# Performance work log

Measured on AMD Instinct MI355X. Metric: run time of the kernel, lower is better.

Reference implementation:

```python
import jax, jax.numpy as jnp
import numpy as np

D_MODEL = 256
N_HEADS = 8
N_LEVELS = 4
N_POINTS = 4
D_FFN = 1024
HW = 128
LQ = HW * HW
LIN = N_LEVELS * LQ
BATCH = 2
HEAD_DIM = D_MODEL // N_HEADS
SPATIAL = [(HW, HW)] * N_LEVELS  # static (H, W) per level
EPS = 1e-5


def _layer_norm(x, g, b):
    m = jnp.mean(x, axis=-1, keepdims=True)
    v = jnp.mean(jnp.square(x - m), axis=-1, keepdims=True)
    return (x - m) * jax.lax.rsqrt(v + EPS) * g + b


def _gather(v, idx):
    # v: (N, heads, HW, hd); idx: (N, heads, Lq, P) -> (N, heads, Lq, P, hd)
    N, Hh, Lq, P = idx.shape
    out = jnp.take_along_axis(v, idx.reshape(N, Hh, Lq * P)[..., None], axis=2)
    return out.reshape(N, Hh, Lq, P, -1)


def _ms_deform_attn_core(value, loc, attn):
    # value: (N, Lin, heads, hd); loc: (N, Lq, heads, L, P, 2) in [0,1]; attn: (N, Lq, heads, L, P)
    N, _, Hh, hd = value.shape
    Lq = loc.shape[1]
    out = jnp.zeros((N, Hh, Lq, hd), value.dtype)
    start = 0
    for l, (H, W) in enumerate(SPATIAL):
        v = value[:, start:start + H * W].transpose(0, 2, 1, 3)  # (N, heads, H*W, hd)
        start += H * W
        ll = loc[:, :, :, l].transpose(0, 2, 1, 3, 4)  # (N, heads, Lq, P, 2)
        # F.grid_sample(align_corners=False, padding_mode='zeros') on grid 2*loc-1:
        # pixel coord = loc * size - 0.5
        x = ll[..., 0] * W - 0.5
        y = ll[..., 1] * H - 0.5
        x0 = jnp.floor(x)
        y0 = jnp.floor(y)
        wx = x - x0
        wy = y - y0
        x0i = x0.astype(jnp.int32)
        y0i = y0.astype(jnp.int32)
        acc = jnp.zeros((N, Hh, Lq, N_POINTS, hd), value.dtype)
        for dy, wyc in ((0, 1.0 - wy), (1, wy)):
            for dx, wxc in ((0, 1.0 - wx), (1, wx)):
                xi = x0i + dx
                yi = y0i + dy
                valid = (xi >= 0) & (xi < W) & (yi >= 0) & (yi < H)
                idx = jnp.clip(yi, 0, H - 1) * W + jnp.clip(xi, 0, W - 1)
                g = _gather(v, idx)
                w = (wxc * wyc * valid).astype(value.dtype)
                acc = acc + g * w[..., None]
        aw = attn[:, :, :, l].transpose(0, 2, 1, 3)  # (N, heads, Lq, P)
        out = out + jnp.sum(acc * aw[..., None], axis=3)
    return out.transpose(0, 2, 1, 3).reshape(N, Lq, Hh * hd)


def _forward(cur_src, src_all, pos, reference_points, spatial_shape,
             W_off, b_off, W_attn, b_attn, W_val, b_val, W_out, b_out,
             gamma1, beta1, W1, b1, W2, b2, gamma2, beta2):
    N, Lq, d = cur_src.shape
    q = cur_src + pos[:, -1]                      # with_pos_embed(cur_src, pos[-1])
    inp = src_all + pos.reshape(N, -1, d)         # with_pos_embed(src_all, cat(pos, 1))
    value = (inp @ W_val + b_val).reshape(N, -1, N_HEADS, HEAD_DIM)
    off = (q @ W_off + b_off).reshape(N, Lq, N_HEADS, N_LEVELS, N_POINTS, 2)
    attn = (q @ W_attn + b_attn).reshape(N, Lq, N_HEADS, N_LEVELS * N_POINTS)
    attn = jax.nn.softmax(attn, axis=-1).reshape(N, Lq, N_HEADS, N_LEVELS, N_POINTS)
    # offset_normalizer = stack([W, H], -1)
    normalizer = jnp.stack([spatial_shape[..., 1], spatial_shape[..., 0]], -1).astype(cur_src.dtype)
    loc = reference_points[:, :, None, :, None, :] + off / normalizer[None, None, None, :, None, :]
    src2 = _ms_deform_attn_core(value, loc, attn) @ W_out + b_out
    src = _layer_norm(cur_src + src2, gamma1, beta1)   # dropout is identity in eval
    ffn = jax.nn.relu(src @ W1 + b1) @ W2 + b2
    return _layer_norm(src + ffn, gamma2, beta2)


def setup_inputs():
    key = jax.random.key(0)
    ks = jax.random.split(key, 16)
    s = 0.02
    f32 = jnp.float32
    return {
        "cur_src": jax.random.normal(ks[0], (BATCH, LQ, D_MODEL), f32),
        "src_all": jax.random.normal(ks[1], (BATCH, LIN, D_MODEL), f32),
        "pos": jax.random.normal(ks[2], (BATCH, N_LEVELS, LQ, D_MODEL), f32),
        "reference_points": jax.random.uniform(ks[3], (BATCH, LQ, N_LEVELS, 2), f32),
        "spatial_shape": jnp.array(SPATIAL, dtype=jnp.int32),
        "level_start_index": (jnp.arange(N_LEVELS) * LQ).astype(jnp.int32),
        "W_off": jax.random.normal(ks[4], (D_MODEL, N_HEADS * N_LEVELS * N_POINTS * 2), f32) * s,
        "b_off": jax.random.normal(ks[5], (N_HEADS * N_LEVELS * N_POINTS * 2,), f32) * 0.5,
        "W_attn": jax.random.normal(ks[6], (D_MODEL, N_HEADS * N_LEVELS * N_POINTS), f32) * s,
        "b_attn": jnp.zeros((N_HEADS * N_LEVELS * N_POINTS,), f32),
        "W_val": jax.random.normal(ks[7], (D_MODEL, D_MODEL), f32) * s,
        "b_val": jnp.zeros((D_MODEL,), f32),
        "W_out": jax.random.normal(ks[8], (D_MODEL, D_MODEL), f32) * s,
        "b_out": jnp.zeros((D_MODEL,), f32),
        "gamma1": jnp.ones((D_MODEL,), f32),
        "beta1": jnp.zeros((D_MODEL,), f32),
        "W1": jax.random.normal(ks[9], (D_MODEL, D_FFN), f32) * s,
        "b1": jnp.zeros((D_FFN,), f32),
        "W2": jax.random.normal(ks[10], (D_FFN, D_MODEL), f32) * s,
        "b2": jnp.zeros((D_MODEL,), f32),
        "gamma2": jnp.ones((D_MODEL,), f32),
        "beta2": jnp.zeros((D_MODEL,), f32),
    }


def reference(cur_src, src_all, pos, reference_points, spatial_shape, level_start_index,
              W_off, b_off, W_attn, b_attn, W_val, b_val, W_out, b_out,
              gamma1, beta1, W1, b1, W2, b2, gamma2, beta2):
    return _forward(cur_src, src_all, pos, reference_points, spatial_shape,
                    W_off, b_off, W_attn, b_attn, W_val, b_val, W_out, b_out,
                    gamma1, beta1, W1, b1, W2, b2, gamma2, beta2)
```

## Files before the change

kernel.cpp:

```cpp
#include <hip/hip_runtime.h>

#define LQN   16384
#define LINN  65536

typedef __attribute__((ext_vector_type(8))) short bf16x8;
typedef __attribute__((ext_vector_type(4))) float f32x4;
typedef __attribute__((ext_vector_type(4))) unsigned short bf16x4;

__device__ __forceinline__ unsigned short f2bf(float f) {
  unsigned u = __float_as_uint(f);
  u += 0x7FFFu + ((u >> 16) & 1u);
  return (unsigned short)(u >> 16);
}

__global__ __launch_bounds__(256) void wtrans_kernel(const float* __restrict__ W,
                                                     unsigned short* __restrict__ Wt,
                                                     int K, int N) {
  int idx = blockIdx.x * 256 + threadIdx.x;
  int n = idx / K, k = idx - n * K;
  Wt[idx] = f2bf(W[(size_t)k * N + n]);
}

__global__ __launch_bounds__(256) void q_kernel(const float* __restrict__ cur,
                                                const float* __restrict__ pos,
                                                unsigned short* __restrict__ q) {
  size_t i = (size_t)blockIdx.x * 256 + threadIdx.x;
  size_t row = i >> 6;
  int n = (int)(row >> 14), lq = (int)(row & 16383);
  float4 a = ((const float4*)cur)[i];
  float4 b = ((const float4*)pos)[(((size_t)n * 4 + 3) * LQN + lq) * 64 + (i & 63)];
  bf16x4 o;
  o.x = f2bf(a.x + b.x); o.y = f2bf(a.y + b.y);
  o.z = f2bf(a.z + b.z); o.w = f2bf(a.w + b.w);
  ((bf16x4*)q)[i] = o;
}

template <int A_BF16, int HAS_A2, int DO_RELU, int OUT_BF16>
__global__ __launch_bounds__(256) void gemm_kernel(
    const void* __restrict__ Ap, const float* __restrict__ A2,
    const unsigned short* __restrict__ Bt, const float* __restrict__ bias,
    void* __restrict__ Cp, int M, int N, int K) {
  __shared__ unsigned short As[128][72];
  __shared__ unsigned short Bs[128][72];
  const int tid = threadIdx.x;
  const int m0 = blockIdx.x * 128, n0 = blockIdx.y * 128;
  const int wave = tid >> 6, lane = tid & 63;
  const int wm = (wave >> 1) * 64, wn = (wave & 1) * 64;
  const int l15 = lane & 15, quad = lane >> 4;

  f32x4 acc[4][4];
#pragma unroll
  for (int i = 0; i < 4; i++)
#pragma unroll
    for (int j = 0; j < 4; j++)
#pragma unroll
      for (int r = 0; r < 4; r++) acc[i][j][r] = 0.f;

  for (int k0 = 0; k0 < K; k0 += 64) {
    if (A_BF16) {
      const unsigned short* A = (const unsigned short*)Ap;
#pragma unroll
      for (int j = 0; j < 4; j++) {
        int c = tid + j * 256;
        int row = c >> 3, ks = (c & 7) * 8;
        bf16x8 v = *(const bf16x8*)(A + (size_t)(m0 + row) * K + k0 + ks);
        *(bf16x8*)&As[row][ks] = v;
      }
    } else {
      const float* A = (const float*)Ap;
#pragma unroll
      for (int j = 0; j < 8; j++) {
        int c = tid + j * 256;
        int row = c >> 4, ks = (c & 15) * 4;
        float4 v = *(const float4*)(A + (size_t)(m0 + row) * K + k0 + ks);
        if (HAS_A2) {
          float4 w = *(const float4*)(A2 + (size_t)(m0 + row) * K + k0 + ks);
          v.x += w.x; v.y += w.y; v.z += w.z; v.w += w.w;
        }
        bf16x4 b;
        b.x = f2bf(v.x); b.y = f2bf(v.y); b.z = f2bf(v.z); b.w = f2bf(v.w);
        *(bf16x4*)&As[row][ks] = b;
      }
    }
#pragma unroll
    for (int j = 0; j < 4; j++) {
      int c = tid + j * 256;
      int row = c >> 3, ks = (c & 7) * 8;
      bf16x8 v = *(const bf16x8*)(Bt + (size_t)(n0 + row) * K + k0 + ks);
      *(bf16x8*)&Bs[row][ks] = v;
    }
    __syncthreads();
#pragma unroll
    for (int kk = 0; kk < 64; kk += 32) {
      bf16x8 af[4], bfr[4];
#pragma unroll
      for (int i = 0; i < 4; i++) af[i] = *(const bf16x8*)&As[wm + i * 16 + l15][kk + quad * 8];
#pragma unroll
      for (int j = 0; j < 4; j++) bfr[j] = *(const bf16x8*)&Bs[wn + j * 16 + l15][kk + quad * 8];
#pragma unroll
      for (int i = 0; i < 4; i++)
#pragma unroll
        for (int j = 0; j < 4; j++)
          acc[i][j] = __builtin_amdgcn_mfma_f32_16x16x32_bf16(af[i], bfr[j], acc[i][j], 0, 0, 0);
    }
    __syncthreads();
  }
#pragma unroll
  for (int i = 0; i < 4; i++) {
#pragma unroll
    for (int j = 0; j < 4; j++) {
      const int col = n0 + wn + j * 16 + l15;
      const float bv = bias[col];
#pragma unroll
      for (int r = 0; r < 4; r++) {
        const int row = m0 + wm + i * 16 + quad * 4 + r;
        float v = acc[i][j][r] + bv;
        if (DO_RELU) v = fmaxf(v, 0.f);
        if (OUT_BF16)
          ((unsigned short*)Cp)[(size_t)row * N + col] = f2bf(v);
        else
          ((float*)Cp)[(size_t)row * N + col] = v;
      }
    }
  }
}

__global__ __launch_bounds__(256) void sample_kernel(
    const unsigned short* __restrict__ value, const float* __restrict__ offs,
    const float* __restrict__ attnl, const float* __restrict__ refp,
    unsigned int* __restrict__ attn_out) {
  const int tid = threadIdx.x;
  const int sub = tid >> 4;
  const int c = tid & 15;
  const int g = blockIdx.x * 16 + sub;
  const int n = g >> 17;
  const int nl = g >> 3;
  const int h = g & 7;

  const float* lg = attnl + (size_t)nl * 128 + h * 16;
  float e[16];
  float mx = -1e30f;
#pragma unroll
  for (int i = 0; i < 16; i++) { e[i] = lg[i]; mx = fmaxf(mx, e[i]); }
  float s = 0.f;
#pragma unroll
  for (int i = 0; i < 16; i++) { e[i] = __expf(e[i] - mx); s += e[i]; }
  const float inv = 1.f / s;

  const int pt = c;
  const int pl = pt >> 2;
  const float ox = offs[((size_t)g * 16 + pt) * 2 + 0];
  const float oy = offs[((size_t)g * 16 + pt) * 2 + 1];
  const float rx = refp[((size_t)nl * 4 + pl) * 2 + 0];
  const float ry = refp[((size_t)nl * 4 + pl) * 2 + 1];
  const float x = fmaf(rx, 128.f, ox - 0.5f);
  const float y = fmaf(ry, 128.f, oy - 0.5f);
  const float xf = floorf(x), yf = floorf(y);
  const float fx = x - xf, fy = y - yf;
  const int x0 = (int)xf, y0 = (int)yf;
  const float aw = e[pt] * inv;
  const int xc0 = min(max(x0, 0), 127), xc1 = min(max(x0 + 1, 0), 127);
  const int yc0 = min(max(y0, 0), 127), yc1 = min(max(y0 + 1, 0), 127);
  float wx0 = (x0 >= 0 && x0 <= 127) ? (1.f - fx) : 0.f;
  float wx1 = (x0 >= -1 && x0 <= 126) ? fx : 0.f;
  float wy0 = ((y0 >= 0 && y0 <= 127) ? (1.f - fy) : 0.f) * aw;
  float wy1 = ((y0 >= -1 && y0 <= 126) ? fy : 0.f) * aw;
  const int packed = xc0 | (xc1 << 7) | (yc0 << 14) | (yc1 << 21);

  const unsigned int* base0 =
      (const unsigned int*)value + (((size_t)n * LINN) * 8 + h) * 16 + c;

  float a0 = 0.f, a1 = 0.f;
#pragma unroll
  for (int p = 0; p < 16; p++) {
    const int pk = __shfl(packed, p, 16);
    const float w_x0 = __shfl(wx0, p, 16);
    const float w_x1 = __shfl(wx1, p, 16);
    const float w_y0 = __shfl(wy0, p, 16);
    const float w_y1 = __shfl(wy1, p, 16);
    const unsigned int* bl = base0 + (size_t)(p >> 2) * (LQN * 128);
    const int X0 = pk & 127, X1 = (pk >> 7) & 127;
    const int Y0 = (pk >> 14) & 127, Y1 = (pk >> 21) & 127;
    const unsigned v00 = bl[(Y0 * 128 + X0) * 128];
    const unsigned v01 = bl[(Y0 * 128 + X1) * 128];
    const unsigned v10 = bl[(Y1 * 128 + X0) * 128];
    const unsigned v11 = bl[(Y1 * 128 + X1) * 128];
    const float w00 = w_x0 * w_y0, w01 = w_x1 * w_y0;
    const float w10 = w_x0 * w_y1, w11 = w_x1 * w_y1;
    a0 = fmaf(w00, __uint_as_float(v00 << 16), a0);
    a1 = fmaf(w00, __uint_as_float(v00 & 0xFFFF0000u), a1);
    a0 = fmaf(w01, __uint_as_float(v01 << 16), a0);
    a1 = fmaf(w01, __uint_as_float(v01 & 0xFFFF0000u), a1);
    a0 = fmaf(w10, __uint_as_float(v10 << 16), a0);
    a1 = fmaf(w10, __uint_as_float(v10 & 0xFFFF0000u), a1);
    a0 = fmaf(w11, __uint_as_float(v11 << 16), a0);
    a1 = fmaf(w11, __uint_as_float(v11 & 0xFFFF0000u), a1);
  }
  attn_out[(size_t)g * 16 + c] = (unsigned)f2bf(a0) | ((unsigned)f2bf(a1) << 16);
}

__global__ __launch_bounds__(64) void ln_kernel(const float* __restrict__ x1,
                                                const float* __restrict__ x2,
                                                const float* __restrict__ gamma,
                                                const float* __restrict__ beta,
                                                float* __restrict__ out) {
  const int row = blockIdx.x, lane = threadIdx.x;
  float4 a = ((const float4*)(x1 + (size_t)row * 256))[lane];
  float4 b = ((const float4*)(x2 + (size_t)row * 256))[lane];
  float v0 = a.x + b.x, v1 = a.y + b.y, v2 = a.z + b.z, v3 = a.w + b.w;
  float s1 = v0 + v1 + v2 + v3;
  float s2 = v0 * v0 + v1 * v1 + v2 * v2 + v3 * v3;
#pragma unroll
  for (int o = 1; o < 64; o <<= 1) { s1 += __shfl_xor(s1, o); s2 += __shfl_xor(s2, o); }
  const float mean = s1 * (1.f / 256.f);
  const float var = s2 * (1.f / 256.f) - mean * mean;
  const float rstd = rsqrtf(var + 1e-5f);
  float4 gm = ((const float4*)gamma)[lane];
  float4 bt = ((const float4*)beta)[lane];
  float4 o4;
  o4.x = (v0 - mean) * rstd * gm.x + bt.x;
  o4.y = (v1 - mean) * rstd * gm.y + bt.y;
  o4.z = (v2 - mean) * rstd * gm.z + bt.z;
  o4.w = (v3 - mean) * rstd * gm.w + bt.w;
  ((float4*)(out + (size_t)row * 256))[lane] = o4;
}

extern "C" void kernel_launch(void* const* d_in, const int* in_sizes, int n_in,
                              void* d_out, int out_size, void* d_ws, size_t ws_size,
                              hipStream_t stream) {
  (void)in_sizes; (void)n_in; (void)out_size; (void)ws_size;
  const float* cur_src = (const float*)d_in[0];
  const float* src_all = (const float*)d_in[1];
  const float* pos     = (const float*)d_in[2];
  const float* refp    = (const float*)d_in[3];
  const float* W_off   = (const float*)d_in[6];
  const float* b_off   = (const float*)d_in[7];
  const float* W_attn  = (const float*)d_in[8];
  const float* b_attn  = (const float*)d_in[9];
  const float* W_val   = (const float*)d_in[10];
  const float* b_val   = (const float*)d_in[11];
  const float* W_out   = (const float*)d_in[12];
  const float* b_out   = (const float*)d_in[13];
  const float* gamma1  = (const float*)d_in[14];
  const float* beta1   = (const float*)d_in[15];
  const float* W1      = (const float*)d_in[16];
  const float* b1      = (const float*)d_in[17];
  const float* W2      = (const float*)d_in[18];
  const float* b2      = (const float*)d_in[19];
  const float* gamma2  = (const float*)d_in[20];
  const float* beta2   = (const float*)d_in[21];
  float* out = (float*)d_out;

  char* ws = (char*)d_ws;
  unsigned short* value = (unsigned short*)(ws + 0);
  unsigned short* qbuf  = (unsigned short*)(ws + 67108864);
  float* offbuf         = (float*)(ws + 83886080);
  float* attnl          = (float*)(ws + 117440512);
  unsigned short* attno = (unsigned short*)(ws + 134217728);
  float* src2           = (float*)(ws + 150994944);
  float* srcb           = (float*)(ws + 184549376);
  unsigned short* wt    = (unsigned short*)(ws + 218103808);
  unsigned short* wt_val  = wt;
  unsigned short* wt_off  = wt + 65536;
  unsigned short* wt_attn = wt + 131072;
  unsigned short* wt_out  = wt + 163840;
  unsigned short* wt_1    = wt + 229376;
  unsigned short* wt_2    = wt + 491520;

  wtrans_kernel<<<256, 256, 0, stream>>>(W_val, wt_val, 256, 256);
  wtrans_kernel<<<256, 256, 0, stream>>>(W_off, wt_off, 256, 256);
  wtrans_kernel<<<128, 256, 0, stream>>>(W_attn, wt_attn, 256, 128);
  wtrans_kernel<<<256, 256, 0, stream>>>(W_out, wt_out, 256, 256);
  wtrans_kernel<<<1024, 256, 0, stream>>>(W1, wt_1, 256, 1024);
  wtrans_kernel<<<1024, 256, 0, stream>>>(W2, wt_2, 1024, 256);

  q_kernel<<<8192, 256, 0, stream>>>(cur_src, pos, qbuf);

  gemm_kernel<0, 1, 0, 1><<<dim3(1024, 2), 256, 0, stream>>>(
      src_all, pos, wt_val, b_val, value, 131072, 256, 256);
  gemm_kernel<1, 0, 0, 0><<<dim3(256, 2), 256, 0, stream>>>(
      qbuf, nullptr, wt_off, b_off, offbuf, 32768, 256, 256);
  gemm_kernel<1, 0, 0, 0><<<dim3(256, 1), 256, 0, stream>>>(
      qbuf, nullptr, wt_attn, b_attn, attnl, 32768, 128, 256);
  sample_kernel<<<16384, 256, 0, stream>>>(value, offbuf, attnl, refp,
                                           (unsigned int*)attno);
  gemm_kernel<1, 0, 0, 0><<<dim3(256, 2), 256, 0, stream>>>(
      attno, nullptr, wt_out, b_out, src2, 32768, 256, 256);
  ln_kernel<<<32768, 64, 0, stream>>>(cur_src, src2, gamma1, beta1, srcb);
  gemm_kernel<0, 0, 1, 1><<<dim3(256, 8), 256, 0, stream>>>(
      srcb, nullptr, wt_1, b1, value, 32768, 1024, 256);
  gemm_kernel<1, 0, 0, 0><<<dim3(256, 2), 256, 0, stream>>>(
      value, nullptr, wt_2, b2, offbuf, 32768, 256, 1024);
  ln_kernel<<<32768, 64, 0, stream>>>(srcb, offbuf, gamma2, beta2, out);
}
```

Measured before the change: 696.3 us.

## Batch weight transposes, issue GEMM loads early, emit bf16 from layernorm

Merges the six weight-transpose launches into one kernel that picks its matrix by index range. In the GEMM, all global loads for A and B are issued into registers before any shared-memory store, so more memory requests are in flight per tile. The layernorm now packs four rows per 256-thread block and can also write a bf16 copy, which the FFN1 GEMM reads directly instead of converting fp32 inside its load loop. The cost is more registers in the GEMM and an extra bf16 buffer write in the first layernorm.

```diff
diff --git a/kernel.cpp b/kernel.cpp
--- a/kernel.cpp
+++ b/kernel.cpp
@@ -13,12 +13,24 @@
   return (unsigned short)(u >> 16);
 }
 
-__global__ __launch_bounds__(256) void wtrans_kernel(const float* __restrict__ W,
-                                                     unsigned short* __restrict__ Wt,
-                                                     int K, int N) {
+__global__ __launch_bounds__(256) void wtrans6_kernel(
+    const float* __restrict__ Wv, const float* __restrict__ Wo,
+    const float* __restrict__ Wa, const float* __restrict__ Wu,
+    const float* __restrict__ W1, const float* __restrict__ W2,
+    unsigned short* __restrict__ wt) {
   int idx = blockIdx.x * 256 + threadIdx.x;
-  int n = idx / K, k = idx - n * K;
-  Wt[idx] = f2bf(W[(size_t)k * N + n]);
+  const float* W; int K, N, base;
+  if (idx < 131072) {
+    if (idx < 65536) { W = Wv; K = 256; N = 256; base = 0; }
+    else             { W = Wo; K = 256; N = 256; base = 65536; }
+  } else if (idx < 229376) {
+    if (idx < 163840) { W = Wa; K = 256; N = 128; base = 131072; }
+    else              { W = Wu; K = 256; N = 256; base = 163840; }
+  } else if (idx < 491520) { W = W1; K = 256; N = 1024; base = 229376; }
+  else                     { W = W2; K = 1024; N = 256; base = 491520; }
+  int local = idx - base;
+  int n = local / K, k = local - n * K;
+  wt[idx] = f2bf(W[(size_t)k * N + n]);
 }
 
 __global__ __launch_bounds__(256) void q_kernel(const float* __restrict__ cur,
@@ -59,35 +71,73 @@
   for (int k0 = 0; k0 < K; k0 += 64) {
     if (A_BF16) {
       const unsigned short* A = (const unsigned short*)Ap;
-#pragma unroll
-      for (int j = 0; j < 4; j++) {
-        int c = tid + j * 256;
-        int row = c >> 3, ks = (c & 7) * 8;
-        bf16x8 v = *(const bf16x8*)(A + (size_t)(m0 + row) * K + k0 + ks);
-        *(bf16x8*)&As[row][ks] = v;
+      bf16x8 va[4], vb[4];
+#pragma unroll
+      for (int j = 0; j < 4; j++) {
+        int c = tid + j * 256;
+        int row = c >> 3, ks = (c & 7) * 8;
+        va[j] = *(const bf16x8*)(A + (size_t)(m0 + row) * K + k0 + ks);
+      }
+#pragma unroll
+      for (int j = 0; j < 4; j++) {
+        int c = tid + j * 256;
+        int row = c >> 3, ks = (c & 7) * 8;
+        vb[j] = *(const bf16x8*)(Bt + (size_t)(n0 + row) * K + k0 + ks);
+      }
+#pragma unroll
+      for (int j = 0; j < 4; j++) {
+        int c = tid + j * 256;
+        int row = c >> 3, ks = (c & 7) * 8;
+        *(bf16x8*)&As[row][ks] = va[j];
+      }
+#pragma unroll
+      for (int j = 0; j < 4; j++) {
+        int c = tid + j * 256;
+        int row = c >> 3, ks = (c & 7) * 8;
+        *(bf16x8*)&Bs[row][ks] = vb[j];
       }
     } else {
       const float* A = (const float*)Ap;
+      float4 va[8], vw[8];
+      bf16x8 vb[4];
 #pragma unroll
       for (int j = 0; j < 8; j++) {
         int c = tid + j * 256;
         int row = c >> 4, ks = (c & 15) * 4;
-        float4 v = *(const float4*)(A + (size_t)(m0 + row) * K + k0 + ks);
+        va[j] = *(const float4*)(A + (size_t)(m0 + row) * K + k0 + ks);
+      }
+      if (HAS_A2) {
+#pragma unroll
+        for (int j = 0; j < 8; j++) {
+          int c = tid + j * 256;
+          int row = c >> 4, ks = (c & 15) * 4;
+          vw[j] = *(const float4*)(A2 + (size_t)(m0 + row) * K + k0 + ks);
+        }
+      }
+#pragma unroll
+      for (int j = 0; j < 4; j++) {
+        int c = tid + j * 256;
+        int row = c >> 3, ks = (c & 7) * 8;
+        vb[j] = *(const bf16x8*)(Bt + (size_t)(n0 + row) * K + k0 + ks);
+      }
+#pragma unroll
+      for (int j = 0; j < 8; j++) {
+        int c = tid + j * 256;
+        int row = c >> 4, ks = (c & 15) * 4;
+        float4 v = va[j];
         if (HAS_A2) {
-          float4 w = *(const float4*)(A2 + (size_t)(m0 + row) * K + k0 + ks);
-          v.x += w.x; v.y += w.y; v.z += w.z; v.w += w.w;
+          v.x += vw[j].x; v.y += vw[j].y; v.z += vw[j].z; v.w += vw[j].w;
         }
         bf16x4 b;
         b.x = f2bf(v.x); b.y = f2bf(v.y); b.z = f2bf(v.z); b.w = f2bf(v.w);
         *(bf16x4*)&As[row][ks] = b;
       }
-    }
-#pragma unroll
-    for (int j = 0; j < 4; j++) {
-      int c = tid + j * 256;
-      int row = c >> 3, ks = (c & 7) * 8;
-      bf16x8 v = *(const bf16x8*)(Bt + (size_t)(n0 + row) * K + k0 + ks);
-      *(bf16x8*)&Bs[row][ks] = v;
+#pragma unroll
+      for (int j = 0; j < 4; j++) {
+        int c = tid + j * 256;
+        int row = c >> 3, ks = (c & 7) * 8;
+        *(bf16x8*)&Bs[row][ks] = vb[j];
+      }
     }
     __syncthreads();
 #pragma unroll
@@ -199,12 +249,15 @@
   attn_out[(size_t)g * 16 + c] = (unsigned)f2bf(a0) | ((unsigned)f2bf(a1) << 16);
 }
 
-__global__ __launch_bounds__(64) void ln_kernel(const float* __restrict__ x1,
-                                                const float* __restrict__ x2,
-                                                const float* __restrict__ gamma,
-                                                const float* __restrict__ beta,
-                                                float* __restrict__ out) {
-  const int row = blockIdx.x, lane = threadIdx.x;
+template <int EMIT_BF16>
+__global__ __launch_bounds__(256) void ln_kernel(const float* __restrict__ x1,
+                                                 const float* __restrict__ x2,
+                                                 const float* __restrict__ gamma,
+                                                 const float* __restrict__ beta,
+                                                 float* __restrict__ out,
+                                                 unsigned short* __restrict__ outb) {
+  const int row = blockIdx.x * 4 + (threadIdx.x >> 6);
+  const int lane = threadIdx.x & 63;
   float4 a = ((const float4*)(x1 + (size_t)row * 256))[lane];
   float4 b = ((const float4*)(x2 + (size_t)row * 256))[lane];
   float v0 = a.x + b.x, v1 = a.y + b.y, v2 = a.z + b.z, v3 = a.w + b.w;
@@ -223,6 +276,11 @@
   o4.z = (v2 - mean) * rstd * gm.z + bt.z;
   o4.w = (v3 - mean) * rstd * gm.w + bt.w;
   ((float4*)(out + (size_t)row * 256))[lane] = o4;
+  if (EMIT_BF16) {
+    bf16x4 ob;
+    ob.x = f2bf(o4.x); ob.y = f2bf(o4.y); ob.z = f2bf(o4.z); ob.w = f2bf(o4.w);
+    ((bf16x4*)(outb + (size_t)row * 256))[lane] = ob;
+  }
 }
 
 extern "C" void kernel_launch(void* const* d_in, const int* in_sizes, int n_in,
@@ -266,13 +324,9 @@
   unsigned short* wt_out  = wt + 163840;
   unsigned short* wt_1    = wt + 229376;
   unsigned short* wt_2    = wt + 491520;
-
-  wtrans_kernel<<<256, 256, 0, stream>>>(W_val, wt_val, 256, 256);
-  wtrans_kernel<<<256, 256, 0, stream>>>(W_off, wt_off, 256, 256);
-  wtrans_kernel<<<128, 256, 0, stream>>>(W_attn, wt_attn, 256, 128);
-  wtrans_kernel<<<256, 256, 0, stream>>>(W_out, wt_out, 256, 256);
-  wtrans_kernel<<<1024, 256, 0, stream>>>(W1, wt_1, 256, 1024);
-  wtrans_kernel<<<1024, 256, 0, stream>>>(W2, wt_2, 1024, 256);
+  unsigned short* srcb_bf = (unsigned short*)attnl;
+
+  wtrans6_kernel<<<2944, 256, 0, stream>>>(W_val, W_off, W_attn, W_out, W1, W2, wt);
 
   q_kernel<<<8192, 256, 0, stream>>>(cur_src, pos, qbuf);
 
@@ -286,10 +340,10 @@
                                            (unsigned int*)attno);
   gemm_kernel<1, 0, 0, 0><<<dim3(256, 2), 256, 0, stream>>>(
       attno, nullptr, wt_out, b_out, src2, 32768, 256, 256);
-  ln_kernel<<<32768, 64, 0, stream>>>(cur_src, src2, gamma1, beta1, srcb);
-  gemm_kernel<0, 0, 1, 1><<<dim3(256, 8), 256, 0, stream>>>(
-      srcb, nullptr, wt_1, b1, value, 32768, 1024, 256);
+  ln_kernel<1><<<8192, 256, 0, stream>>>(cur_src, src2, gamma1, beta1, srcb, srcb_bf);
+  gemm_kernel<1, 0, 1, 1><<<dim3(256, 8), 256, 0, stream>>>(
+      srcb_bf, nullptr, wt_1, b1, value, 32768, 1024, 256);
   gemm_kernel<1, 0, 0, 0><<<dim3(256, 2), 256, 0, stream>>>(
       value, nullptr, wt_2, b2, offbuf, 32768, 256, 1024);
-  ln_kernel<<<32768, 64, 0, stream>>>(srcb, offbuf, gamma2, beta2, out);
-}
+  ln_kernel<0><<<8192, 256, 0, stream>>>(srcb, offbuf, gamma2, beta2, out, nullptr);
+}
```

After: 684.5 us. No clear change (-1.7%).
